# Optimization experiments

Hardware: AMD Instinct MI355X
Metric: run time of the kernel (lower is better)

## Reference

```python
import jax, jax.numpy as jnp
import numpy as np

DIM = 128
GROUPS = [1, 2, 2, 3]


def setup_inputs() -> dict:
    key = jax.random.key(0)
    ks = jax.random.split(key, 8)
    c = DIM
    def p(k, shape, scale=0.02):
        return jax.random.normal(k, shape, dtype=jnp.float32) * scale
    return {
        "x": jax.random.normal(ks[0], (8, c, 128, 128), dtype=jnp.float32),
        "temperature": jnp.ones((4, 1, 1), dtype=jnp.float32),
        "w_qkv": p(ks[1], (3 * c, c)),            # Conv2d(dim, 3*dim, 1), bias=False
        "w_dw": p(ks[2], (3 * c, 1, 3, 3)),        # depthwise 3x3, groups=3*dim
        "w_proj": p(ks[3], (c, c)),                # Conv2d(dim, dim, 1), bias=False
        "w_gate": p(ks[4], (c, c)),                # Intra gatingConv (Conv1d k=1)
        "b_gate": jnp.zeros((c,), jnp.float32),
        "w_down": p(ks[5], (c // 2, c)),           # Intra down
        "b_down": jnp.zeros((c // 2,), jnp.float32),
        "w_up": p(ks[6], (c, c // 2)),             # Intra up
        "b_up": jnp.zeros((c,), jnp.float32),
    }


def _group_sizes(c):
    total = sum(GROUPS)
    sizes = [int(r / total * c) for r in GROUPS]
    sizes[-1] += c - sum(sizes)
    return sizes


def _forward(x, temperature, w_qkv, w_dw, w_proj, w_gate, b_gate,
             w_down, b_down, w_up, b_up):
    b, c, h, w = x.shape
    L = h * w
    # qkv = dwconv3x3(conv1x1(x))
    qkv = jnp.einsum('bchw,oc->bohw', x, w_qkv)
    qkv = jax.lax.conv_general_dilated(
        qkv, w_dw, (1, 1), 'SAME', feature_group_count=3 * c,
        dimension_numbers=('NCHW', 'OIHW', 'NCHW'))
    q, k, v = jnp.split(qkv.reshape(b, 3 * c, L), 3, axis=1)
    # ReGroup: sort channels by mean q activation (descending), split into groups
    channel_mean = q.mean(axis=(0, 2))            # (c,)
    idx = jnp.argsort(-channel_mean)
    q, k, v = q[:, idx], k[:, idx], v[:, idx]
    sizes = _group_sizes(c)
    outs, caches, cache_means = [], [], []
    start = 0
    for i, g in enumerate(sizes):
        qg = q[:, start:start + g]
        kg = k[:, start:start + g]
        vg = v[:, start:start + g]
        start += g
        qn = qg / jnp.maximum(jnp.linalg.norm(qg, axis=-1, keepdims=True), 1e-12)
        kn = kg / jnp.maximum(jnp.linalg.norm(kg, axis=-1, keepdims=True), 1e-12)
        attn = jax.nn.softmax(
            jnp.einsum('bcl,bdl->bcd', qn, kn) * temperature[i, 0, 0], axis=-1)
        outs.append(jnp.einsum('bcd,bdl->bcl', attn, vg))   # (b, g, L)
        tc = jax.lax.stop_gradient(qn + kn)                 # detached cache
        caches.append(tc)
        # per-group mean over L, channel-tiled/padded to c (for cache update)
        gm = tc.mean(axis=-1)                               # (b, g)
        rep = max(1, c // g)
        gm = jnp.tile(gm, (1, rep))
        gm = gm[:, :c] if gm.shape[1] >= c else jnp.pad(gm, ((0, 0), (0, c - gm.shape[1])))
        cache_means.append(gm)
    out_all = jnp.concatenate(outs, axis=1)       # (b, c, L)
    tmp_caches = jnp.concatenate(caches, axis=1)  # (b, c, L)
    # CalculateCurrentLayerCache: bilinear upsample of (1,1) map == broadcast
    s = int(L ** 0.5 + 0.9999)
    acc = sum(cache_means) / float(len(cache_means))        # (b, c)
    qv_cache = jnp.broadcast_to((acc * 0.9)[:, :, None, None], (b, c, s, s))
    # Intra cache modulation: gated = gelu(conv(x1+x2)) * (x1+x2); up(down(gated))
    sxy = out_all + tmp_caches
    gating = jax.nn.gelu(jnp.einsum('bcl,oc->bol', sxy, w_gate) + b_gate[:, None],
                         approximate=False)
    gated = gating * sxy
    mod = jnp.einsum('bcl,oc->bol', gated, w_down) + b_down[:, None]
    mod = jnp.einsum('bcl,oc->bol', mod, w_up) + b_up[:, None]
    out_all = mod + out_all
    out_all = jnp.einsum('bchw,oc->bohw', out_all.reshape(b, c, h, w), w_proj)
    return out_all, qv_cache


def reference(x, temperature, w_qkv, w_dw, w_proj, w_gate, b_gate,
              w_down, b_down, w_up, b_up):
    return _forward(x, temperature, w_qkv, w_dw, w_proj, w_gate, b_gate,
                    w_down, b_down, w_up, b_up)
```

## Files before the change

kernel.cpp:

```cpp
#include <hip/hip_runtime.h>
#include <math.h>

#define B_ 8
#define C_ 128
#define O3_ 384
#define H_ 128
#define W_ 128
#define L_ 16384
#define NS_ 64
#define MAXP_ 2304

typedef float f32x4 __attribute__((ext_vector_type(4)));
typedef short bf16x8 __attribute__((ext_vector_type(8)));

static __device__ __forceinline__ ushort f2bf(float f) {
    uint u = __float_as_uint(f);
    u += 0x7fffu + ((u >> 16) & 1u);
    return (ushort)(u >> 16);
}
static __device__ __forceinline__ float bf2f(ushort h) {
    return __uint_as_float(((uint)h) << 16);
}

__global__ __launch_bounds__(256) void wsplit_k(
    const float* __restrict__ wa, const float* __restrict__ wb,
    const float* __restrict__ wc, const float* __restrict__ wd,
    short* __restrict__ ha, short* __restrict__ la,
    short* __restrict__ hb, short* __restrict__ lb,
    short* __restrict__ hc, short* __restrict__ lc,
    short* __restrict__ hd, short* __restrict__ ld)
{
    const int sel = blockIdx.y;
    const float* w = sel == 0 ? wa : (sel == 1 ? wb : (sel == 2 ? wc : wd));
    short* ph = sel == 0 ? ha : (sel == 1 ? hb : (sel == 2 ? hc : hd));
    short* pl = sel == 0 ? la : (sel == 1 ? lb : (sel == 2 ? lc : ld));
    const int n = sel == 0 ? 49152 : (sel == 1 ? 16384 : 8192);
    const int i = blockIdx.x * 256 + threadIdx.x;
    if (i < n) {
        float v = w[i];
        ushort h = f2bf(v);
        ph[i] = (short)h;
        pl[i] = (short)f2bf(v - bf2f(h));
    }
}

__global__ __launch_bounds__(256) void wsplit1_k(const float* __restrict__ w,
    short* __restrict__ ph, short* __restrict__ pl, int n)
{
    const int i = blockIdx.x * 256 + threadIdx.x;
    if (i < n) {
        float v = w[i];
        ushort h = f2bf(v);
        ph[i] = (short)h;
        pl[i] = (short)f2bf(v - bf2f(h));
    }
}

__global__ __launch_bounds__(256) void transp_k(const float* __restrict__ x,
    short* __restrict__ xhi, short* __restrict__ xlo)
{
    __shared__ float t[128][33];
    const int b = blockIdx.y;
    const int l0 = blockIdx.x * 32;
    const int tid = threadIdx.x;
    {
        const int c = tid >> 1, half = tid & 1;
        const float* src = x + ((size_t)b * C_ + c) * L_ + l0 + half * 16;
#pragma unroll
        for (int u = 0; u < 4; u++) {
            float4 v = *reinterpret_cast<const float4*>(src + u * 4);
            t[c][half * 16 + u * 4 + 0] = v.x;
            t[c][half * 16 + u * 4 + 1] = v.y;
            t[c][half * 16 + u * 4 + 2] = v.z;
            t[c][half * 16 + u * 4 + 3] = v.w;
        }
    }
    __syncthreads();
    {
        const int l = tid >> 3, strip = tid & 7;
        uint hi[8], lo[8];
#pragma unroll
        for (int i = 0; i < 8; i++) {
            float a0 = t[strip * 16 + 2 * i][l], a1 = t[strip * 16 + 2 * i + 1][l];
            ushort h0 = f2bf(a0), h1 = f2bf(a1);
            ushort g0 = f2bf(a0 - bf2f(h0)), g1 = f2bf(a1 - bf2f(h1));
            hi[i] = (uint)h0 | ((uint)h1 << 16);
            lo[i] = (uint)g0 | ((uint)g1 << 16);
        }
        size_t ob = ((size_t)b * L_ + l0 + l) * C_ + strip * 16;
        uint4* ph = reinterpret_cast<uint4*>(xhi + ob);
        uint4* pl = reinterpret_cast<uint4*>(xlo + ob);
        ph[0] = *reinterpret_cast<uint4*>(&hi[0]);
        ph[1] = *reinterpret_cast<uint4*>(&hi[4]);
        pl[0] = *reinterpret_cast<uint4*>(&lo[0]);
        pl[1] = *reinterpret_cast<uint4*>(&lo[4]);
    }
}

template<int KD, int OT, int MODE>
__global__ __launch_bounds__(256) void mgemm_k(
    const short* __restrict__ Whi, const short* __restrict__ Wlo,
    const float* __restrict__ bias,
    const short* __restrict__ Ahi, const short* __restrict__ Alo,
    const float* __restrict__ E0,
    float* __restrict__ Yf, short* __restrict__ Yhi, short* __restrict__ Ylo)
{
    constexpr int WC = OT / 64;
    constexpr int WR = 4 / WC;
    constexpr int LT = WR * 64;
    constexpr int T  = KD / 32;
    constexpr int BBYTES = OT * KD * 2;
    constexpr int CB = (OT * KD) / 2048;
    __shared__ __align__(16) char sBh[BBYTES];
    __shared__ __align__(16) char sBl[BBYTES];

    const int tid = threadIdx.x;
    const int lane = tid & 63;
    const int wid = tid >> 6;
    const int wr = wid / WC, wc = wid % WC;
    const int oB = blockIdx.x * OT;
    const int lB = blockIdx.y * LT;
    const int ON = gridDim.x * OT;
    const int b  = blockIdx.z;
    const int ln15 = lane & 15, lg = lane >> 4;
    const int m0B = ln15 & 3;
    const int m1B = (ln15 >> 2) & (T - 1);

#pragma unroll
    for (int p = 0; p < CB; p++) {
        const int id = tid + p * 256;
        const int row = id / (KD / 8), cs = id % (KD / 8);
        const int tt = cs >> 2, ks = cs & 3;
        const size_t src = (size_t)(oB + row) * KD + cs * 8;
        const int dst = row * (KD * 2) + ((tt ^ ((row >> 2) & (T - 1))) * 64)
                      + ((ks ^ (row & 3)) << 4);
        *reinterpret_cast<uint4*>(sBh + dst) = *reinterpret_cast<const uint4*>(Whi + src);
        *reinterpret_cast<uint4*>(sBl + dst) = *reinterpret_cast<const uint4*>(Wlo + src);
    }

    f32x4 acc[4][4];
#pragma unroll
    for (int m = 0; m < 4; m++)
#pragma unroll
        for (int n = 0; n < 4; n++)
#pragma unroll
            for (int r = 0; r < 4; r++) acc[m][n][r] = 0.f;

    const size_t arow = ((size_t)b * L_ + lB + wr * 64 + ln15) * KD + lg * 8;

    bf16x8 A0h[4], A0l[4], A1h[4], A1l[4];
    auto ldA = [&](bf16x8* Ah, bf16x8* Al, int t) {
#pragma unroll
        for (int m = 0; m < 4; m++) {
            const size_t g = arow + (size_t)(m * 16) * KD + t * 32;
            Ah[m] = *reinterpret_cast<const bf16x8*>(Ahi + g);
            Al[m] = *reinterpret_cast<const bf16x8*>(Alo + g);
        }
    };

    ldA(A0h, A0l, 0);
    if (T > 1) ldA(A1h, A1l, 1);
    __syncthreads();

#pragma unroll
    for (int t = 0; t < T; t++) {
        bf16x8 Bh[4], Bl[4];
#pragma unroll
        for (int n = 0; n < 4; n++) {
            const int row = wc * 64 + n * 16 + ln15;
            const int bb = row * (KD * 2) + ((t ^ m1B) * 64) + ((lg ^ m0B) << 4);
            Bh[n] = *reinterpret_cast<const bf16x8*>(sBh + bb);
            Bl[n] = *reinterpret_cast<const bf16x8*>(sBl + bb);
        }
        const bf16x8* Ah = (t & 1) ? A1h : A0h;
        const bf16x8* Al = (t & 1) ? A1l : A0l;
#pragma unroll
        for (int n = 0; n < 4; n++)
#pragma unroll
            for (int m = 0; m < 4; m++) {
                acc[m][n] = __builtin_amdgcn_mfma_f32_16x16x32_bf16(Ah[m], Bh[n], acc[m][n], 0, 0, 0);
                acc[m][n] = __builtin_amdgcn_mfma_f32_16x16x32_bf16(Ah[m], Bl[n], acc[m][n], 0, 0, 0);
                acc[m][n] = __builtin_amdgcn_mfma_f32_16x16x32_bf16(Al[m], Bh[n], acc[m][n], 0, 0, 0);
            }
        if (t + 2 < T) {
            if (t & 1) ldA(A1h, A1l, t + 2);
            else       ldA(A0h, A0l, t + 2);
        }
    }

#pragma unroll
    for (int m = 0; m < 4; m++) {
        const int l = lB + wr * 64 + m * 16 + lg * 4;
#pragma unroll
        for (int n = 0; n < 4; n++) {
            const int o = oB + wc * 64 + n * 16 + ln15;
            if constexpr (MODE == 4) {
                float4 r4 = {acc[m][n][0], acc[m][n][1], acc[m][n][2], acc[m][n][3]};
                *reinterpret_cast<float4*>(&Yf[((size_t)b * ON + o) * L_ + l]) = r4;
            } else {
                float bv = bias[o];
#pragma unroll
                for (int r = 0; r < 4; r++) {
                    size_t yi = ((size_t)b * L_ + l + r) * ON + o;
                    float a = acc[m][n][r] + bv;
                    if constexpr (MODE == 1) {
                        float sxy = bf2f((ushort)Ahi[yi]) + bf2f((ushort)Alo[yi]);
                        a = 0.5f * a * (1.f + erff(a * 0.70710678118654752f)) * sxy;
                    }
                    if constexpr (MODE == 3) a += E0[yi];
                    ushort h = f2bf(a);
                    ushort g = f2bf(a - bf2f(h));
                    Yhi[yi] = (short)h;
                    Ylo[yi] = (short)g;
                }
            }
        }
    }
}

__global__ __launch_bounds__(256) void dwconv_k(const float* __restrict__ in,
    const float* __restrict__ wdw, float* __restrict__ outp,
    float* __restrict__ sumq, float* __restrict__ sumk,
    float* __restrict__ ssq, float* __restrict__ ssk)
{
    const int ch = blockIdx.x, b = blockIdx.y;
    const int tid = threadIdx.x;
    const int tx = tid & 31, band = tid >> 5;
    const int x0 = tx * 4;
    const int y0 = band * 16;
    const size_t base = ((size_t)b * O3_ + ch) * L_;
    const float* wp = wdw + ch * 9;
    float w0 = wp[0], w1 = wp[1], w2 = wp[2], w3 = wp[3], w4 = wp[4],
          w5 = wp[5], w6 = wp[6], w7 = wp[7], w8 = wp[8];

    float s1 = 0.f, s2 = 0.f;
    float b0[6], b1[6], b2[6];

    auto loadrow = [&](int gy, float* r) {
        if ((unsigned)gy < (unsigned)H_) {
            const float* rp = in + base + (size_t)gy * W_;
            float4 m = *reinterpret_cast<const float4*>(rp + x0);
            r[0] = (x0 > 0) ? rp[x0 - 1] : 0.f;
            r[1] = m.x; r[2] = m.y; r[3] = m.z; r[4] = m.w;
            r[5] = (x0 < W_ - 4) ? rp[x0 + 4] : 0.f;
        } else {
            r[0] = r[1] = r[2] = r[3] = r[4] = r[5] = 0.f;
        }
    };
    auto conv3 = [&](const float* ra, const float* rb, const float* rc, int yy) {
        float o0 = ra[0]*w0 + ra[1]*w1 + ra[2]*w2 + rb[0]*w3 + rb[1]*w4 + rb[2]*w5 + rc[0]*w6 + rc[1]*w7 + rc[2]*w8;
        float o1 = ra[1]*w0 + ra[2]*w1 + ra[3]*w2 + rb[1]*w3 + rb[2]*w4 + rb[3]*w5 + rc[1]*w6 + rc[2]*w7 + rc[3]*w8;
        float o2 = ra[2]*w0 + ra[3]*w1 + ra[4]*w2 + rb[2]*w3 + rb[3]*w4 + rb[4]*w5 + rc[2]*w6 + rc[3]*w7 + rc[4]*w8;
        float o3 = ra[3]*w0 + ra[4]*w1 + ra[5]*w2 + rb[3]*w3 + rb[4]*w4 + rb[5]*w5 + rc[3]*w6 + rc[4]*w7 + rc[5]*w8;
        float4 o4 = {o0, o1, o2, o3};
        *reinterpret_cast<float4*>(&outp[base + (size_t)(y0 + yy) * W_ + x0]) = o4;
        s1 += (o0 + o1) + (o2 + o3);
        s2 += o0*o0 + o1*o1 + o2*o2 + o3*o3;
    };

    loadrow(y0 - 1, b0);
    loadrow(y0,     b1);
#pragma unroll
    for (int y3 = 0; y3 < 15; y3 += 3) {
        loadrow(y0 + y3 + 1, b2); conv3(b0, b1, b2, y3);
        loadrow(y0 + y3 + 2, b0); conv3(b1, b2, b0, y3 + 1);
        loadrow(y0 + y3 + 3, b1); conv3(b2, b0, b1, y3 + 2);
    }
    loadrow(y0 + 16, b2); conv3(b0, b1, b2, 15);

    __shared__ float r1[256], r2[256];
    if (ch < 256) {
        r1[tid] = s1; r2[tid] = s2;
        __syncthreads();
        for (int st = 128; st > 0; st >>= 1) {
            if (tid < st) { r1[tid] += r1[tid + st]; r2[tid] += r2[tid + st]; }
            __syncthreads();
        }
        if (tid == 0) {
            if (ch < 128) { sumq[b * 128 + ch] = r1[0]; ssq[b * 128 + ch] = r2[0]; }
            else          { sumk[b * 128 + ch - 128] = r1[0]; ssk[b * 128 + ch - 128] = r2[0]; }
        }
    }
}

__global__ void combine_k(const float* __restrict__ sumq, const float* __restrict__ sumk,
    const float* __restrict__ ssq, const float* __restrict__ ssk,
    int* __restrict__ idxp, float* __restrict__ rqc, float* __restrict__ rkc,
    float* __restrict__ gm)
{
    const int t = threadIdx.x;
    __shared__ double cms[128];
    double s = 0.0;
    for (int b = 0; b < B_; b++) s += (double)sumq[b * 128 + t];
    cms[t] = s;
    float rqv[B_], rkv[B_];
    for (int b = 0; b < B_; b++) {
        rqv[b] = 1.f / fmaxf(sqrtf(ssq[b * 128 + t]), 1e-12f);
        rkv[b] = 1.f / fmaxf(sqrtf(ssk[b * 128 + t]), 1e-12f);
        rqc[b * 128 + t] = rqv[b];
        rkc[b * 128 + t] = rkv[b];
    }
    __syncthreads();
    const double mv = cms[t];
    int r = 0;
    for (int j = 0; j < 128; j++) {
        double o = cms[j];
        if (o > mv || (o == mv && j < t)) r++;
    }
    idxp[r] = t;
    for (int b = 0; b < B_; b++)
        gm[b * 128 + r] = (rqv[b] * sumq[b * 128 + t] + rkv[b] * sumk[b * 128 + t]) * (1.0f / L_);
}

template<int G>
__global__ __launch_bounds__(256) void score_k(const float* __restrict__ dw, const int* __restrict__ idxp,
    int start, int gi, float* __restrict__ spart)
{
    constexpr int TS = G / 16;
    const int split = blockIdx.x, b = blockIdx.y;
    const int tid = threadIdx.x, tx = tid & 15, ty = tid >> 4;
    __shared__ float sQ[G][66];
    __shared__ float sK[G][66];
    __shared__ int sc[G];
    if (tid < G) sc[tid] = idxp[start + tid];
    __syncthreads();

    float acc[TS][TS];
#pragma unroll
    for (int i = 0; i < TS; i++)
#pragma unroll
        for (int j = 0; j < TS; j++) acc[i][j] = 0.f;

    const int l0 = split * (L_ / NS_);
    constexpr int LPT = (G * 64) / 256;
    for (int chk = 0; chk < L_ / NS_; chk += 64) {
#pragma unroll
        for (int i = 0; i < LPT; i++) {
            int id = tid + i * 256;
            int row = id >> 6, lc = id & 63;
            size_t base = ((size_t)b * O3_ + sc[row]) * L_ + l0 + chk + lc;
            sQ[row][lc] = dw[base];
            sK[row][lc] = dw[base + (size_t)128 * L_];
        }
        __syncthreads();
#pragma unroll
        for (int kk = 0; kk < 64; kk++) {
            float qv[TS], kv[TS];
#pragma unroll
            for (int j = 0; j < TS; j++) { qv[j] = sQ[ty * TS + j][kk]; kv[j] = sK[tx * TS + j][kk]; }
#pragma unroll
            for (int i = 0; i < TS; i++)
#pragma unroll
                for (int j = 0; j < TS; j++)
                    acc[i][j] = fmaf(qv[i], kv[j], acc[i][j]);
        }
        __syncthreads();
    }
    float* op = spart + (((size_t)(b * 4 + gi)) * NS_ + split) * MAXP_;
#pragma unroll
    for (int i = 0; i < TS; i++)
#pragma unroll
        for (int j = 0; j < TS; j++)
            op[(ty * TS + i) * G + tx * TS + j] = acc[i][j];
}

__global__ __launch_bounds__(256) void softmax_k(const float* __restrict__ spart,
    const float* __restrict__ rqc, const float* __restrict__ rkc, const int* __restrict__ idxp,
    const float* __restrict__ temp, float* __restrict__ attn)
{
    const int gi = blockIdx.x, b = blockIdx.y;
    const int g = (gi == 0) ? 16 : (gi == 3 ? 48 : 32);
    const int start = (gi == 0) ? 0 : (gi == 1 ? 16 : (gi == 2 ? 48 : 80));
    __shared__ float S[MAXP_];
    __shared__ int sidx[48];
    if (threadIdx.x < g) sidx[threadIdx.x] = idxp[start + threadIdx.x];
    __syncthreads();
    const float tv = temp[gi];
    for (int p = threadIdx.x; p < g * g; p += 256) {
        float s = 0.f;
        const float* sp = spart + ((size_t)(b * 4 + gi)) * NS_ * MAXP_ + p;
        for (int k = 0; k < NS_; k++) s += sp[(size_t)k * MAXP_];
        int cc = p / g, dd = p - cc * g;
        S[p] = s * rqc[b * 128 + sidx[cc]] * rkc[b * 128 + sidx[dd]] * tv;
    }
    __syncthreads();
    const int wv = threadIdx.x >> 6, lane = threadIdx.x & 63;
    for (int r = wv; r < g; r += 4) {
        float val = (lane < g) ? S[r * g + lane] : -1e30f;
        float mx = val;
        for (int m = 32; m > 0; m >>= 1) mx = fmaxf(mx, __shfl_xor(mx, m));
        float e = (lane < g) ? expf(val - mx) : 0.f;
        float sum = e;
        for (int m = 32; m > 0; m >>= 1) sum += __shfl_xor(sum, m);
        if (lane < g) attn[((size_t)(b * 4 + gi)) * MAXP_ + r * g + lane] = e / sum;
    }
}

template<int G>
__global__ __launch_bounds__(256) void av3_k(const float* __restrict__ dw, const int* __restrict__ idxp,
    const float* __restrict__ rqc, const float* __restrict__ rkc,
    const float* __restrict__ attn, int start, int gi,
    float* __restrict__ outallT, short* __restrict__ sxyhi, short* __restrict__ sxylo)
{
    constexpr int C4 = G / 4;
    constexpr int GP = G + 1;
    const int b = blockIdx.y;
    const int lB = blockIdx.x * 64;
    const int tid = threadIdx.x;
    __shared__ float sA[G * GP];
    __shared__ float sV[64][GP];
    __shared__ int cv[G];
    __shared__ float rqs[G], rks[G];
    if (tid < G) {
        int c0 = idxp[start + tid];
        cv[tid] = c0;
        rqs[tid] = rqc[b * 128 + c0];
        rks[tid] = rkc[b * 128 + c0];
    }
    for (int p = tid; p < G * G; p += 256) {
        int cc = p / G, dd = p - cc * G;
        sA[cc * GP + dd] = attn[((size_t)(b * 4 + gi)) * MAXP_ + p];
    }
    __syncthreads();
    for (int idx = tid; idx < 64 * G; idx += 256) {
        int l = idx & 63, d = idx >> 6;
        sV[l][d] = dw[((size_t)b * O3_ + 256 + cv[d]) * L_ + lB + l];
    }
    __syncthreads();
    const int strip = tid & 3, l = tid >> 2;
    float acc[C4];
#pragma unroll
    for (int j = 0; j < C4; j++) acc[j] = 0.f;
    for (int d = 0; d < G; d++) {
        float vd = sV[l][d];
#pragma unroll
        for (int j = 0; j < C4; j++)
            acc[j] = fmaf(sA[(strip * C4 + j) * GP + d], vd, acc[j]);
    }
    const size_t ob = ((size_t)b * L_ + lB + l) * C_ + start + strip * C4;
    float sv[C4];
#pragma unroll
    for (int j = 0; j < C4; j++) {
        int c = strip * C4 + j;
        float q = dw[((size_t)b * O3_ + cv[c]) * L_ + lB + l];
        float k = dw[((size_t)b * O3_ + 128 + cv[c]) * L_ + lB + l];
        sv[j] = acc[j] + rqs[c] * q + rks[c] * k;
    }
#pragma unroll
    for (int j = 0; j < C4; j += 4) {
        float4 o4 = {acc[j], acc[j + 1], acc[j + 2], acc[j + 3]};
        *reinterpret_cast<float4*>(&outallT[ob + j]) = o4;
    }
#pragma unroll
    for (int j = 0; j < C4; j += 2) {
        ushort h0 = f2bf(sv[j]), h1 = f2bf(sv[j + 1]);
        ushort g0 = f2bf(sv[j] - bf2f(h0)), g1 = f2bf(sv[j + 1] - bf2f(h1));
        *reinterpret_cast<uint*>(&sxyhi[ob + j]) = (uint)h0 | ((uint)h1 << 16);
        *reinterpret_cast<uint*>(&sxylo[ob + j]) = (uint)g0 | ((uint)g1 << 16);
    }
}

__global__ __launch_bounds__(256) void qvc_k(const float* __restrict__ gm, float* __restrict__ outq)
{
    const int cpos = blockIdx.x, b = blockIdx.y;
    const float* g = gm + b * 128;
    float v = g[cpos & 15] + g[16 + (cpos & 31)] + g[48 + (cpos & 31)];
    if (cpos < 96) v += g[80 + (cpos % 48)];
    v *= 0.225f;
    float4 vv = {v, v, v, v};
    float4* op = reinterpret_cast<float4*>(outq + ((size_t)b * C_ + cpos) * L_);
    for (int i = threadIdx.x; i < L_ / 4; i += 256) op[i] = vv;
}

extern "C" void kernel_launch(void* const* d_in, const int* in_sizes, int n_in,
                              void* d_out, int out_size, void* d_ws, size_t ws_size,
                              hipStream_t stream)
{
    const float* x     = (const float*)d_in[0];
    const float* temp  = (const float*)d_in[1];
    const float* wqkv  = (const float*)d_in[2];
    const float* wdw   = (const float*)d_in[3];
    const float* wproj = (const float*)d_in[4];
    const float* wgate = (const float*)d_in[5];
    const float* bgate = (const float*)d_in[6];
    const float* wdown = (const float*)d_in[7];
    const float* bdown = (const float*)d_in[8];
    const float* wup   = (const float*)d_in[9];
    const float* bup   = (const float*)d_in[10];
    float* out = (float*)d_out;
    float* ws  = (float*)d_ws;

    float* qkvCL = ws;
    float* dwCL  = ws + 50331648ull;
    short* xThi  = (short*)(ws + 50331648ull);
    short* xTlo  = xThi + 16777216ull;
    float* outallT = ws;
    short* sxyhi   = (short*)(ws + 16777216ull);
    short* sxylo   = sxyhi + 16777216ull;
    short* gatedhi = (short*)(ws + 33554432ull);
    short* gatedlo = gatedhi + 16777216ull;
    short* mod1hi  = (short*)(ws + 16777216ull);
    short* mod1lo  = mod1hi + 8388608ull;
    short* out2hi  = (short*)(ws + 33554432ull);
    short* out2lo  = out2hi + 16777216ull;
    short* wprojh  = (short*)(ws + 25165824ull);
    short* wprojl  = wprojh + 16384ull;

    float* spart = out;
    float* attn  = out + 4718592ull;
    float* sumq  = out + 4800000ull;
    float* sumk  = out + 4801024ull;
    float* ssq   = out + 4802048ull;
    float* ssk   = out + 4803072ull;
    float* rqc   = out + 4804096ull;
    float* rkc   = out + 4805120ull;
    float* gm    = out + 4806144ull;
    int*   idxp  = (int*)(out + 4807168ull);
    short* wqkvh = (short*)(out + 4900000ull);
    short* wqkvl = (short*)(out + 4924576ull);
    short* wgateh= (short*)(out + 4949152ull);
    short* wgatel= (short*)(out + 4957344ull);
    short* wdownh= (short*)(out + 4965536ull);
    short* wdownl= (short*)(out + 4969632ull);
    short* wuph  = (short*)(out + 4973728ull);
    short* wupl  = (short*)(out + 4977824ull);

    wsplit_k<<<dim3(192, 4), 256, 0, stream>>>(wqkv, wgate, wdown, wup,
        wqkvh, wqkvl, wgateh, wgatel, wdownh, wdownl, wuph, wupl);
    transp_k<<<dim3(512, 8), 256, 0, stream>>>(x, xThi, xTlo);
    mgemm_k<128, 64, 4><<<dim3(6, 64, 8), 256, 0, stream>>>(
        wqkvh, wqkvl, nullptr, xThi, xTlo, nullptr, qkvCL, nullptr, nullptr);
    dwconv_k<<<dim3(384, 8), 256, 0, stream>>>(qkvCL, wdw, dwCL, sumq, sumk, ssq, ssk);
    combine_k<<<1, 128, 0, stream>>>(sumq, sumk, ssq, ssk, idxp, rqc, rkc, gm);
    score_k<16><<<dim3(NS_, 8), 256, 0, stream>>>(dwCL, idxp, 0, 0, spart);
    score_k<32><<<dim3(NS_, 8), 256, 0, stream>>>(dwCL, idxp, 16, 1, spart);
    score_k<32><<<dim3(NS_, 8), 256, 0, stream>>>(dwCL, idxp, 48, 2, spart);
    score_k<48><<<dim3(NS_, 8), 256, 0, stream>>>(dwCL, idxp, 80, 3, spart);
    softmax_k<<<dim3(4, 8), 256, 0, stream>>>(spart, rqc, rkc, idxp, temp, attn);
    av3_k<16><<<dim3(256, 8), 256, 0, stream>>>(dwCL, idxp, rqc, rkc, attn, 0, 0, outallT, sxyhi, sxylo);
    av3_k<32><<<dim3(256, 8), 256, 0, stream>>>(dwCL, idxp, rqc, rkc, attn, 16, 1, outallT, sxyhi, sxylo);
    av3_k<32><<<dim3(256, 8), 256, 0, stream>>>(dwCL, idxp, rqc, rkc, attn, 48, 2, outallT, sxyhi, sxylo);
    av3_k<48><<<dim3(256, 8), 256, 0, stream>>>(dwCL, idxp, rqc, rkc, attn, 80, 3, outallT, sxyhi, sxylo);
    mgemm_k<128, 64, 1><<<dim3(2, 64, 8), 256, 0, stream>>>(
        wgateh, wgatel, bgate, sxyhi, sxylo, nullptr, nullptr, gatedhi, gatedlo);
    qvc_k<<<dim3(128, 8), 256, 0, stream>>>(gm, out + 16777216ull);
    mgemm_k<128, 64, 2><<<dim3(1, 64, 8), 256, 0, stream>>>(
        wdownh, wdownl, bdown, gatedhi, gatedlo, nullptr, nullptr, mod1hi, mod1lo);
    mgemm_k<64, 64, 3><<<dim3(2, 64, 8), 256, 0, stream>>>(
        wuph, wupl, bup, mod1hi, mod1lo, outallT, nullptr, out2hi, out2lo);
    wsplit1_k<<<64, 256, 0, stream>>>(wproj, wprojh, wprojl, 16384);
    mgemm_k<128, 64, 4><<<dim3(2, 64, 8), 256, 0, stream>>>(
        wprojh, wprojl, nullptr, out2hi, out2lo, nullptr, out, nullptr, nullptr);
}
```

Baseline: 793.9 us.

## Fuse gate/down/up/proj GEMM chain into one LDS-resident kernel

```diff
diff --git a/kernel.cpp b/kernel.cpp
--- a/kernel.cpp
+++ b/kernel.cpp
@@ -22,28 +22,6 @@
     return __uint_as_float(((uint)h) << 16);
 }
 
-__global__ __launch_bounds__(256) void wsplit_k(
-    const float* __restrict__ wa, const float* __restrict__ wb,
-    const float* __restrict__ wc, const float* __restrict__ wd,
-    short* __restrict__ ha, short* __restrict__ la,
-    short* __restrict__ hb, short* __restrict__ lb,
-    short* __restrict__ hc, short* __restrict__ lc,
-    short* __restrict__ hd, short* __restrict__ ld)
-{
-    const int sel = blockIdx.y;
-    const float* w = sel == 0 ? wa : (sel == 1 ? wb : (sel == 2 ? wc : wd));
-    short* ph = sel == 0 ? ha : (sel == 1 ? hb : (sel == 2 ? hc : hd));
-    short* pl = sel == 0 ? la : (sel == 1 ? lb : (sel == 2 ? lc : ld));
-    const int n = sel == 0 ? 49152 : (sel == 1 ? 16384 : 8192);
-    const int i = blockIdx.x * 256 + threadIdx.x;
-    if (i < n) {
-        float v = w[i];
-        ushort h = f2bf(v);
-        ph[i] = (short)h;
-        pl[i] = (short)f2bf(v - bf2f(h));
-    }
-}
-
 __global__ __launch_bounds__(256) void wsplit1_k(const float* __restrict__ w,
     short* __restrict__ ph, short* __restrict__ pl, int n)
 {
@@ -97,13 +75,11 @@
     }
 }
 
-template<int KD, int OT, int MODE>
+template<int KD, int OT>
 __global__ __launch_bounds__(256) void mgemm_k(
     const short* __restrict__ Whi, const short* __restrict__ Wlo,
-    const float* __restrict__ bias,
     const short* __restrict__ Ahi, const short* __restrict__ Alo,
-    const float* __restrict__ E0,
-    float* __restrict__ Yf, short* __restrict__ Yhi, short* __restrict__ Ylo)
+    float* __restrict__ Yf)
 {
     constexpr int WC = OT / 64;
     constexpr int WR = 4 / WC;
@@ -194,25 +170,249 @@
 #pragma unroll
         for (int n = 0; n < 4; n++) {
             const int o = oB + wc * 64 + n * 16 + ln15;
-            if constexpr (MODE == 4) {
-                float4 r4 = {acc[m][n][0], acc[m][n][1], acc[m][n][2], acc[m][n][3]};
-                *reinterpret_cast<float4*>(&Yf[((size_t)b * ON + o) * L_ + l]) = r4;
-            } else {
-                float bv = bias[o];
+            float4 r4 = {acc[m][n][0], acc[m][n][1], acc[m][n][2], acc[m][n][3]};
+            *reinterpret_cast<float4*>(&Yf[((size_t)b * ON + o) * L_ + l]) = r4;
+        }
+    }
+}
+
+__global__ __launch_bounds__(256) void fusedmlp_k(
+    const float* __restrict__ Wg, const float* __restrict__ bg,
+    const float* __restrict__ Wd, const float* __restrict__ bd,
+    const float* __restrict__ Wu, const float* __restrict__ bu,
+    const float* __restrict__ Wp,
+    const short* __restrict__ sxyhi, const short* __restrict__ sxylo,
+    const float* __restrict__ outallT, float* __restrict__ out)
+{
+    constexpr int STR = 136;
+    __shared__ short aH[128 * STR];
+    __shared__ short aL[128 * STR];
+    const int tid = threadIdx.x, lane = tid & 63, wid = tid >> 6;
+    const int wr = wid >> 1, wc = wid & 1;
+    const int b = blockIdx.y;
+    const int lB = blockIdx.x * 128;
+    const int ln15 = lane & 15, lg = lane >> 4;
+    const int koff = lg * 8;
+
+    for (int p = tid; p < 2048; p += 256) {
+        int l = p >> 4, c8 = (p & 15) * 8;
+        size_t g = ((size_t)b * L_ + lB + l) * C_ + c8;
+        *reinterpret_cast<bf16x8*>(&aH[l * STR + c8]) = *reinterpret_cast<const bf16x8*>(&sxyhi[g]);
+        *reinterpret_cast<bf16x8*>(&aL[l * STR + c8]) = *reinterpret_cast<const bf16x8*>(&sxylo[g]);
+    }
+    __syncthreads();
+
+    auto ldW = [&](const float* W, int KD, int o, int ko, bf16x8& bh, bf16x8& bl) {
+        const float* p = W + (size_t)o * KD + ko;
+        float4 v0 = *reinterpret_cast<const float4*>(p);
+        float4 v1 = *reinterpret_cast<const float4*>(p + 4);
+        float f[8] = {v0.x, v0.y, v0.z, v0.w, v1.x, v1.y, v1.z, v1.w};
+#pragma unroll
+        for (int i = 0; i < 8; i++) {
+            ushort h = f2bf(f[i]);
+            bh[i] = (short)h;
+            bl[i] = (short)f2bf(f[i] - bf2f(h));
+        }
+    };
+    auto ldA2 = [&](int row, int ko, bf16x8& ah, bf16x8& al) {
+        ah = *reinterpret_cast<const bf16x8*>(&aH[row * STR + ko]);
+        al = *reinterpret_cast<const bf16x8*>(&aL[row * STR + ko]);
+    };
+
+    {
+        f32x4 acc[4][4];
+#pragma unroll
+        for (int m = 0; m < 4; m++)
+#pragma unroll
+            for (int n = 0; n < 4; n++)
+#pragma unroll
+                for (int r = 0; r < 4; r++) acc[m][n][r] = 0.f;
+#pragma unroll
+        for (int t = 0; t < 4; t++) {
+            bf16x8 Ah[4], Al[4], Bh[4], Bl[4];
+#pragma unroll
+            for (int m = 0; m < 4; m++)
+                ldA2(wr * 64 + m * 16 + ln15, t * 32 + koff, Ah[m], Al[m]);
+#pragma unroll
+            for (int n = 0; n < 4; n++)
+                ldW(Wg, 128, wc * 64 + n * 16 + ln15, t * 32 + koff, Bh[n], Bl[n]);
+#pragma unroll
+            for (int n = 0; n < 4; n++)
+#pragma unroll
+                for (int m = 0; m < 4; m++) {
+                    acc[m][n] = __builtin_amdgcn_mfma_f32_16x16x32_bf16(Ah[m], Bh[n], acc[m][n], 0, 0, 0);
+                    acc[m][n] = __builtin_amdgcn_mfma_f32_16x16x32_bf16(Ah[m], Bl[n], acc[m][n], 0, 0, 0);
+                    acc[m][n] = __builtin_amdgcn_mfma_f32_16x16x32_bf16(Al[m], Bh[n], acc[m][n], 0, 0, 0);
+                }
+        }
+#pragma unroll
+        for (int n = 0; n < 4; n++) {
+            const int o = wc * 64 + n * 16 + ln15;
+            const float bv = bg[o];
+#pragma unroll
+            for (int m = 0; m < 4; m++)
 #pragma unroll
                 for (int r = 0; r < 4; r++) {
-                    size_t yi = ((size_t)b * L_ + l + r) * ON + o;
+                    const int l = wr * 64 + m * 16 + lg * 4 + r;
                     float a = acc[m][n][r] + bv;
-                    if constexpr (MODE == 1) {
-                        float sxy = bf2f((ushort)Ahi[yi]) + bf2f((ushort)Alo[yi]);
-                        a = 0.5f * a * (1.f + erff(a * 0.70710678118654752f)) * sxy;
-                    }
-                    if constexpr (MODE == 3) a += E0[yi];
-                    ushort h = f2bf(a);
-                    ushort g = f2bf(a - bf2f(h));
-                    Yhi[yi] = (short)h;
-                    Ylo[yi] = (short)g;
-                }
+                    a = 0.5f * a * (1.f + erff(a * 0.70710678118654752f));
+                    float s = bf2f((ushort)aH[l * STR + o]) + bf2f((ushort)aL[l * STR + o]);
+                    acc[m][n][r] = a * s;
+                }
+        }
+        __syncthreads();
+#pragma unroll
+        for (int n = 0; n < 4; n++) {
+            const int o = wc * 64 + n * 16 + ln15;
+#pragma unroll
+            for (int m = 0; m < 4; m++)
+#pragma unroll
+                for (int r = 0; r < 4; r++) {
+                    const int l = wr * 64 + m * 16 + lg * 4 + r;
+                    float v = acc[m][n][r];
+                    ushort h = f2bf(v);
+                    aH[l * STR + o] = (short)h;
+                    aL[l * STR + o] = (short)f2bf(v - bf2f(h));
+                }
+        }
+        __syncthreads();
+    }
+
+    {
+        f32x4 a2[4][2];
+#pragma unroll
+        for (int m = 0; m < 4; m++)
+#pragma unroll
+            for (int n = 0; n < 2; n++)
+#pragma unroll
+                for (int r = 0; r < 4; r++) a2[m][n][r] = 0.f;
+#pragma unroll
+        for (int t = 0; t < 4; t++) {
+            bf16x8 Ah[4], Al[4], Bh[2], Bl[2];
+#pragma unroll
+            for (int m = 0; m < 4; m++)
+                ldA2(wr * 64 + m * 16 + ln15, t * 32 + koff, Ah[m], Al[m]);
+#pragma unroll
+            for (int n = 0; n < 2; n++)
+                ldW(Wd, 128, wc * 32 + n * 16 + ln15, t * 32 + koff, Bh[n], Bl[n]);
+#pragma unroll
+            for (int n = 0; n < 2; n++)
+#pragma unroll
+                for (int m = 0; m < 4; m++) {
+                    a2[m][n] = __builtin_amdgcn_mfma_f32_16x16x32_bf16(Ah[m], Bh[n], a2[m][n], 0, 0, 0);
+                    a2[m][n] = __builtin_amdgcn_mfma_f32_16x16x32_bf16(Ah[m], Bl[n], a2[m][n], 0, 0, 0);
+                    a2[m][n] = __builtin_amdgcn_mfma_f32_16x16x32_bf16(Al[m], Bh[n], a2[m][n], 0, 0, 0);
+                }
+        }
+        __syncthreads();
+#pragma unroll
+        for (int n = 0; n < 2; n++) {
+            const int o = wc * 32 + n * 16 + ln15;
+            const float bv = bd[o];
+#pragma unroll
+            for (int m = 0; m < 4; m++)
+#pragma unroll
+                for (int r = 0; r < 4; r++) {
+                    const int l = wr * 64 + m * 16 + lg * 4 + r;
+                    float v = a2[m][n][r] + bv;
+                    ushort h = f2bf(v);
+                    aH[l * STR + o] = (short)h;
+                    aL[l * STR + o] = (short)f2bf(v - bf2f(h));
+                }
+        }
+        __syncthreads();
+    }
+
+    {
+        f32x4 a3[4][4];
+#pragma unroll
+        for (int m = 0; m < 4; m++)
+#pragma unroll
+            for (int n = 0; n < 4; n++)
+#pragma unroll
+                for (int r = 0; r < 4; r++) a3[m][n][r] = 0.f;
+#pragma unroll
+        for (int t = 0; t < 2; t++) {
+            bf16x8 Ah[4], Al[4], Bh[4], Bl[4];
+#pragma unroll
+            for (int m = 0; m < 4; m++)
+                ldA2(wr * 64 + m * 16 + ln15, t * 32 + koff, Ah[m], Al[m]);
+#pragma unroll
+            for (int n = 0; n < 4; n++)
+                ldW(Wu, 64, wc * 64 + n * 16 + ln15, t * 32 + koff, Bh[n], Bl[n]);
+#pragma unroll
+            for (int n = 0; n < 4; n++)
+#pragma unroll
+                for (int m = 0; m < 4; m++) {
+                    a3[m][n] = __builtin_amdgcn_mfma_f32_16x16x32_bf16(Ah[m], Bh[n], a3[m][n], 0, 0, 0);
+                    a3[m][n] = __builtin_amdgcn_mfma_f32_16x16x32_bf16(Ah[m], Bl[n], a3[m][n], 0, 0, 0);
+                    a3[m][n] = __builtin_amdgcn_mfma_f32_16x16x32_bf16(Al[m], Bh[n], a3[m][n], 0, 0, 0);
+                }
+        }
+#pragma unroll
+        for (int n = 0; n < 4; n++) {
+            const int o = wc * 64 + n * 16 + ln15;
+            const float bv = bu[o];
+#pragma unroll
+            for (int m = 0; m < 4; m++)
+#pragma unroll
+                for (int r = 0; r < 4; r++) {
+                    const int l = wr * 64 + m * 16 + lg * 4 + r;
+                    a3[m][n][r] += bv + outallT[((size_t)b * L_ + lB + l) * C_ + o];
+                }
+        }
+        __syncthreads();
+#pragma unroll
+        for (int n = 0; n < 4; n++) {
+            const int o = wc * 64 + n * 16 + ln15;
+#pragma unroll
+            for (int m = 0; m < 4; m++)
+#pragma unroll
+                for (int r = 0; r < 4; r++) {
+                    const int l = wr * 64 + m * 16 + lg * 4 + r;
+                    float v = a3[m][n][r];
+                    ushort h = f2bf(v);
+                    aH[l * STR + o] = (short)h;
+                    aL[l * STR + o] = (short)f2bf(v - bf2f(h));
+                }
+        }
+        __syncthreads();
+    }
+
+    {
+        f32x4 a4[4][4];
+#pragma unroll
+        for (int m = 0; m < 4; m++)
+#pragma unroll
+            for (int n = 0; n < 4; n++)
+#pragma unroll
+                for (int r = 0; r < 4; r++) a4[m][n][r] = 0.f;
+#pragma unroll
+        for (int t = 0; t < 4; t++) {
+            bf16x8 Ah[4], Al[4], Bh[4], Bl[4];
+#pragma unroll
+            for (int m = 0; m < 4; m++)
+                ldA2(wr * 64 + m * 16 + ln15, t * 32 + koff, Ah[m], Al[m]);
+#pragma unroll
+            for (int n = 0; n < 4; n++)
+                ldW(Wp, 128, wc * 64 + n * 16 + ln15, t * 32 + koff, Bh[n], Bl[n]);
+#pragma unroll
+            for (int n = 0; n < 4; n++)
+#pragma unroll
+                for (int m = 0; m < 4; m++) {
+                    a4[m][n] = __builtin_amdgcn_mfma_f32_16x16x32_bf16(Ah[m], Bh[n], a4[m][n], 0, 0, 0);
+                    a4[m][n] = __builtin_amdgcn_mfma_f32_16x16x32_bf16(Ah[m], Bl[n], a4[m][n], 0, 0, 0);
+                    a4[m][n] = __builtin_amdgcn_mfma_f32_16x16x32_bf16(Al[m], Bh[n], a4[m][n], 0, 0, 0);
+                }
+        }
+#pragma unroll
+        for (int m = 0; m < 4; m++) {
+            const int l = lB + wr * 64 + m * 16 + lg * 4;
+#pragma unroll
+            for (int n = 0; n < 4; n++) {
+                const int o = wc * 64 + n * 16 + ln15;
+                float4 r4 = {a4[m][n][0], a4[m][n][1], a4[m][n][2], a4[m][n][3]};
+                *reinterpret_cast<float4*>(&out[((size_t)b * C_ + o) * L_ + l]) = r4;
             }
         }
     }
@@ -497,14 +697,6 @@
     float* outallT = ws;
     short* sxyhi   = (short*)(ws + 16777216ull);
     short* sxylo   = sxyhi + 16777216ull;
-    short* gatedhi = (short*)(ws + 33554432ull);
-    short* gatedlo = gatedhi + 16777216ull;
-    short* mod1hi  = (short*)(ws + 16777216ull);
-    short* mod1lo  = mod1hi + 8388608ull;
-    short* out2hi  = (short*)(ws + 33554432ull);
-    short* out2lo  = out2hi + 16777216ull;
-    short* wprojh  = (short*)(ws + 25165824ull);
-    short* wprojl  = wprojh + 16384ull;
 
     float* spart = out;
     float* attn  = out + 4718592ull;
@@ -518,18 +710,11 @@
     int*   idxp  = (int*)(out + 4807168ull);
     short* wqkvh = (short*)(out + 4900000ull);
     short* wqkvl = (short*)(out + 4924576ull);
-    short* wgateh= (short*)(out + 4949152ull);
-    short* wgatel= (short*)(out + 4957344ull);
-    short* wdownh= (short*)(out + 4965536ull);
-    short* wdownl= (short*)(out + 4969632ull);
-    short* wuph  = (short*)(out + 4973728ull);
-    short* wupl  = (short*)(out + 4977824ull);
-
-    wsplit_k<<<dim3(192, 4), 256, 0, stream>>>(wqkv, wgate, wdown, wup,
-        wqkvh, wqkvl, wgateh, wgatel, wdownh, wdownl, wuph, wupl);
+
+    wsplit1_k<<<192, 256, 0, stream>>>(wqkv, wqkvh, wqkvl, 49152);
     transp_k<<<dim3(512, 8), 256, 0, stream>>>(x, xThi, xTlo);
-    mgemm_k<128, 64, 4><<<dim3(6, 64, 8), 256, 0, stream>>>(
-        wqkvh, wqkvl, nullptr, xThi, xTlo, nullptr, qkvCL, nullptr, nullptr);
+    mgemm_k<128, 128><<<dim3(3, 128, 8), 256, 0, stream>>>(
+        wqkvh, wqkvl, xThi, xTlo, qkvCL);
     dwconv_k<<<dim3(384, 8), 256, 0, stream>>>(qkvCL, wdw, dwCL, sumq, sumk, ssq, ssk);
     combine_k<<<1, 128, 0, stream>>>(sumq, sumk, ssq, ssk, idxp, rqc, rkc, gm);
     score_k<16><<<dim3(NS_, 8), 256, 0, stream>>>(dwCL, idxp, 0, 0, spart);
@@ -541,14 +726,8 @@
     av3_k<32><<<dim3(256, 8), 256, 0, stream>>>(dwCL, idxp, rqc, rkc, attn, 16, 1, outallT, sxyhi, sxylo);
     av3_k<32><<<dim3(256, 8), 256, 0, stream>>>(dwCL, idxp, rqc, rkc, attn, 48, 2, outallT, sxyhi, sxylo);
     av3_k<48><<<dim3(256, 8), 256, 0, stream>>>(dwCL, idxp, rqc, rkc, attn, 80, 3, outallT, sxyhi, sxylo);
-    mgemm_k<128, 64, 1><<<dim3(2, 64, 8), 256, 0, stream>>>(
-        wgateh, wgatel, bgate, sxyhi, sxylo, nullptr, nullptr, gatedhi, gatedlo);
     qvc_k<<<dim3(128, 8), 256, 0, stream>>>(gm, out + 16777216ull);
-    mgemm_k<128, 64, 2><<<dim3(1, 64, 8), 256, 0, stream>>>(
-        wdownh, wdownl, bdown, gatedhi, gatedlo, nullptr, nullptr, mod1hi, mod1lo);
-    mgemm_k<64, 64, 3><<<dim3(2, 64, 8), 256, 0, stream>>>(
-        wuph, wupl, bup, mod1hi, mod1lo, outallT, nullptr, out2hi, out2lo);
-    wsplit1_k<<<64, 256, 0, stream>>>(wproj, wprojh, wprojl, 16384);
-    mgemm_k<128, 64, 4><<<dim3(2, 64, 8), 256, 0, stream>>>(
-        wprojh, wprojl, nullptr, out2hi, out2lo, nullptr, out, nullptr, nullptr);
-}
+    fusedmlp_k<<<dim3(128, 8), 256, 0, stream>>>(
+        wgate, bgate, wdown, bdown, wup, bup, wproj,
+        sxyhi, sxylo, outallT, out);
+}
```

Result: no change. 805.6 us (+1.5%).
